# Kernel tuning notes

Hardware: AMD Instinct MI355X
Metric: run time of the kernel (lower is better)

Reference implementation:

```python
import jax, jax.numpy as jnp
import numpy as np

N = 100000      # nodes
E = 1600000     # edges (avg degree 16)
F_IN = 128      # dataset.num_features
H = 64          # hidden_channels
C = 40          # dataset.num_classes
LAYERS = 4      # number_conv_layers
EPS = 1e-12     # F.normalize eps


def _agnn_layer(x, src, dst):
    # AGNNConv with beta=1 (requires_grad=False):
    # alpha_ij = softmax_i( cos(x_i, x_j) ), out_i = sum_j alpha_ij * x_j
    xn = x / jnp.maximum(jnp.linalg.norm(x, axis=1, keepdims=True), EPS)
    logits = jnp.sum(xn[dst] * xn[src], axis=1)                      # [E]
    m = jax.lax.stop_gradient(jax.ops.segment_max(logits, dst, num_segments=N))
    e = jnp.exp(logits - m[dst])
    s = jax.ops.segment_sum(e, dst, num_segments=N)
    alpha = e / s[dst]                                               # [E]
    return jax.ops.segment_sum(alpha[:, None] * x[src], dst, num_segments=N)


def setup_inputs() -> dict:
    key = jax.random.key(0)
    k = jax.random.split(key, 6)
    x = jax.random.normal(k[0], (N, F_IN), dtype=jnp.float32)
    edge_index = jax.random.randint(k[1], (2, E), 0, N, dtype=jnp.int32)
    W1 = jax.random.normal(k[2], (F_IN, H), dtype=jnp.float32) * (1.0 / np.sqrt(F_IN))
    b1 = jnp.zeros((H,), dtype=jnp.float32)
    W2 = jax.random.normal(k[3], (H, C), dtype=jnp.float32) * (1.0 / np.sqrt(H))
    b2 = jnp.zeros((C,), dtype=jnp.float32)
    return {"x": x, "W1": W1, "b1": b1, "W2": W2, "b2": b2, "edge_index": edge_index}


def reference(x, W1, b1, W2, b2, edge_index):
    # add self loops (PyG AGNNConv default)
    loop = jnp.arange(N, dtype=edge_index.dtype)
    src = jnp.concatenate([edge_index[0], loop])
    dst = jnp.concatenate([edge_index[1], loop])
    h = jax.nn.relu(x @ W1 + b1)          # lin1 + relu (dropout p=0 / eval)
    for _ in range(LAYERS):
        h = _agnn_layer(h, src, dst)
    out = h @ W2 + b2                     # lin2
    return jax.nn.log_softmax(out, axis=1)
```

## Files before the change

kernel.cpp:

```cpp
#include <hip/hip_runtime.h>
#include <math.h>

#define F_IN 128
#define H_DIM 64
#define C_OUT 40
#define NBK 391
#define CHUNK 4096
#define XPAD 136
#define PHB 128

typedef _Float16 h8 __attribute__((ext_vector_type(8)));
typedef _Float16 half2t __attribute__((ext_vector_type(2)));
typedef float nf4 __attribute__((ext_vector_type(4)));
typedef _Float16 f16x8 __attribute__((ext_vector_type(8)));
typedef float f32x4 __attribute__((ext_vector_type(4)));

union H8 {
    h8 v;
    half2t p[4];
};

__device__ __forceinline__ float dot8(const H8& a, const H8& b) {
    float d = __builtin_amdgcn_fdot2(a.p[0], b.p[0], 0.0f, false);
    d = __builtin_amdgcn_fdot2(a.p[1], b.p[1], d, false);
    d = __builtin_amdgcn_fdot2(a.p[2], b.p[2], d, false);
    d = __builtin_amdgcn_fdot2(a.p[3], b.p[3], d, false);
    return d;
}

__device__ __forceinline__ float dpp_red8_add(float x) {
    int v = __builtin_bit_cast(int, x);
    x += __builtin_bit_cast(float, __builtin_amdgcn_update_dpp(0, v, 0xB1, 0xF, 0xF, true));
    v = __builtin_bit_cast(int, x);
    x += __builtin_bit_cast(float, __builtin_amdgcn_update_dpp(0, v, 0x4E, 0xF, 0xF, true));
    v = __builtin_bit_cast(int, x);
    x += __builtin_bit_cast(float, __builtin_amdgcn_update_dpp(0, v, 0x141, 0xF, 0xF, true));
    return x;
}


__global__ void __launch_bounds__(256) bphist_kernel(const int* __restrict__ dst,
                                                     int* __restrict__ part, int E) {
    __shared__ int lh[512];
    int tid = threadIdx.x;
    lh[tid] = 0; lh[tid + 256] = 0;
    __syncthreads();
    int slice = (E + PHB - 1) / PHB;
    int lo = blockIdx.x * slice;
    int hi = min(E, lo + slice);
    for (int e = lo + tid; e < hi; e += 256) {
        int d = __builtin_nontemporal_load(&dst[e]);
        atomicAdd(&lh[d >> 8], 1);
    }
    __syncthreads();
    part[blockIdx.x * 512 + tid] = lh[tid];
    part[blockIdx.x * 512 + tid + 256] = lh[tid + 256];
}

__global__ void __launch_bounds__(512) bscan_kernel(const int* __restrict__ part,
                                                    int* __restrict__ bbase,
                                                    int* __restrict__ bcursor, int E) {
    __shared__ int sa[512], sb[512];
    int t = threadIdx.x;
    int v = 0;
#pragma unroll 4
    for (int b = 0; b < PHB; b++) v += part[b * 512 + t];
    sa[t] = v;
    __syncthreads();
    int* pa = sa; int* pb = sb;
#pragma unroll
    for (int off = 1; off < 512; off <<= 1) {
        pb[t] = pa[t] + ((t >= off) ? pa[t - off] : 0);
        __syncthreads();
        int* tmp = pa; pa = pb; pb = tmp;
    }
    if (t < NBK) {
        int excl = pa[t] - v;
        bbase[t] = excl;
        bcursor[t] = excl;
    }
    if (t == 0) bbase[NBK] = E;
}

__global__ void __launch_bounds__(256) binscatter_kernel(const int* __restrict__ src,
                                                         const int* __restrict__ dst,
                                                         int* __restrict__ bcursor,
                                                         unsigned int* __restrict__ pairs, int E) {
    __shared__ unsigned int sp[CHUNK];
    __shared__ unsigned short sbof[CHUNK];
    __shared__ int hist[512];
    __shared__ int scanA[512], scanB[512];
    __shared__ int cur[512];
    __shared__ int gbase[512];
    int tid = threadIdx.x;
    int e0 = blockIdx.x * CHUNK;
    int cnt = min(CHUNK, E - e0);

    int dv[CHUNK / 256], sv[CHUNK / 256];
#pragma unroll
    for (int i = 0; i < CHUNK / 256; i++) {
        int idx = tid + i * 256;
        if (idx < cnt) {
            dv[i] = __builtin_nontemporal_load(&dst[e0 + idx]);
            sv[i] = __builtin_nontemporal_load(&src[e0 + idx]);
        }
    }
    hist[tid] = 0; hist[tid + 256] = 0;
    __syncthreads();
#pragma unroll
    for (int i = 0; i < CHUNK / 256; i++) {
        int idx = tid + i * 256;
        if (idx < cnt) atomicAdd(&hist[dv[i] >> 8], 1);
    }
    __syncthreads();
    scanA[tid] = hist[tid]; scanA[tid + 256] = hist[tid + 256];
    __syncthreads();
    int* pa = scanA; int* pb = scanB;
#pragma unroll
    for (int off = 1; off < 512; off <<= 1) {
        pb[tid] = pa[tid] + ((tid >= off) ? pa[tid - off] : 0);
        int t1 = tid + 256;
        pb[t1] = pa[t1] + ((t1 >= off) ? pa[t1 - off] : 0);
        __syncthreads();
        int* tmp = pa; pa = pb; pb = tmp;
    }
    cur[tid] = pa[tid] - hist[tid];
    cur[tid + 256] = pa[tid + 256] - hist[tid + 256];
    __syncthreads();
#pragma unroll
    for (int i = 0; i < CHUNK / 256; i++) {
        int idx = tid + i * 256;
        if (idx < cnt) {
            int b = dv[i] >> 8;
            int lp = atomicAdd(&cur[b], 1);
            sp[lp] = ((unsigned int)(dv[i] & 255) << 24) | (unsigned int)sv[i];
            sbof[lp] = (unsigned short)b;
        }
    }
    {
        int c0 = hist[tid];
        gbase[tid] = c0 ? atomicAdd(&bcursor[tid], c0) : 0;
        int c1 = hist[tid + 256];
        gbase[tid + 256] = c1 ? atomicAdd(&bcursor[tid + 256], c1) : 0;
    }
    __syncthreads();
    for (int i = tid; i < cnt; i += 256) {
        int b = sbof[i];
        int off_in_b = i - (pa[b] - hist[b]);
        pairs[gbase[b] + off_in_b] = sp[i];
    }
}

__global__ void __launch_bounds__(256) bucketsort_kernel(const unsigned int* __restrict__ pairs,
                                                         const int* __restrict__ bbase,
                                                         int* __restrict__ rowptr,
                                                         int* __restrict__ ssrc, int N, int E) {
    __shared__ int hist[256], scanA[256], scanB[256], cur[256];
    int b = blockIdx.x;
    int tid = threadIdx.x;
    int e0 = bbase[b], e1 = bbase[b + 1];
    hist[tid] = 0;
    __syncthreads();
    for (int e = e0 + tid; e < e1; e += 256) {
        unsigned int p = pairs[e];
        atomicAdd(&hist[p >> 24], 1);
    }
    __syncthreads();
    scanA[tid] = hist[tid];
    __syncthreads();
    int* pa = scanA; int* pb = scanB;
#pragma unroll
    for (int off = 1; off < 256; off <<= 1) {
        pb[tid] = pa[tid] + ((tid >= off) ? pa[tid - off] : 0);
        __syncthreads();
        int* tmp = pa; pa = pb; pb = tmp;
    }
    int excl = pa[tid] - hist[tid];
    int node = (b << 8) + tid;
    if (node < N) rowptr[node] = e0 + excl;
    if (b == NBK - 1 && tid == 0) rowptr[N] = E;
    cur[tid] = e0 + excl;
    __syncthreads();
    for (int e = e0 + tid; e < e1; e += 256) {
        unsigned int p = pairs[e];
        int pos = atomicAdd(&cur[p >> 24], 1);
        ssrc[pos] = (int)(p & 0x00FFFFFFu);
    }
}

__global__ void __launch_bounds__(256) cvtw_kernel(const float* __restrict__ W1,
                                                   _Float16* __restrict__ w1t) {
    int t = blockIdx.x * 256 + threadIdx.x;
    if (t < F_IN * H_DIM) {
        int k = t >> 6, col = t & 63;
        w1t[col * F_IN + k] = (_Float16)W1[t];
    }
}

__global__ void __launch_bounds__(256) lin1_kernel(
        const float* __restrict__ x, const _Float16* __restrict__ w1t,
        const float* __restrict__ b1, _Float16* __restrict__ hnout,
        float* __restrict__ nrmout, int n) {
    __shared__ _Float16 sx[64 * XPAD];
    __shared__ _Float16 sw[64 * XPAD];
    int tid = threadIdx.x;
    int r0 = blockIdx.x * 64;

    for (int ch = tid; ch < 64 * 32; ch += 256) {
        int row = ch >> 5, k4 = (ch & 31) << 2;
        float4 xv = make_float4(0.f, 0.f, 0.f, 0.f);
        if (r0 + row < n) xv = *(const float4*)(x + (size_t)(r0 + row) * F_IN + k4);
        _Float16* p = &sx[row * XPAD + k4];
        p[0] = (_Float16)xv.x; p[1] = (_Float16)xv.y;
        p[2] = (_Float16)xv.z; p[3] = (_Float16)xv.w;
    }
    for (int ch = tid; ch < 64 * 16; ch += 256) {
        int col = ch >> 4, k8 = (ch & 15) << 3;
        *(uint4*)&sw[col * XPAD + k8] = *(const uint4*)(w1t + col * F_IN + k8);
    }
    __syncthreads();

    int w = tid >> 6, lane = tid & 63;
    int q = lane >> 4, c = lane & 15;

    f16x8 afrag[4];
#pragma unroll
    for (int kk = 0; kk < 4; kk++)
        afrag[kk] = *(const f16x8*)&sx[(w * 16 + c) * XPAD + kk * 32 + q * 8];

    f32x4 acc[4] = {{0.f,0.f,0.f,0.f},{0.f,0.f,0.f,0.f},{0.f,0.f,0.f,0.f},{0.f,0.f,0.f,0.f}};
#pragma unroll
    for (int ct = 0; ct < 4; ct++) {
#pragma unroll
        for (int kk = 0; kk < 4; kk++) {
            f16x8 bfrag = *(const f16x8*)&sw[(ct * 16 + c) * XPAD + kk * 32 + q * 8];
            acc[ct] = __builtin_amdgcn_mfma_f32_16x16x32_f16(afrag[kk], bfrag, acc[ct], 0, 0, 0);
        }
    }

    float ss[4] = {0.f, 0.f, 0.f, 0.f};
#pragma unroll
    for (int ct = 0; ct < 4; ct++) {
        float bv = b1[ct * 16 + c];
#pragma unroll
        for (int r = 0; r < 4; r++) {
            float v = fmaxf(acc[ct][r] + bv, 0.0f);
            acc[ct][r] = v;
            ss[r] = fmaf(v, v, ss[r]);
        }
    }
#pragma unroll
    for (int k = 1; k < 16; k <<= 1) {
#pragma unroll
        for (int r = 0; r < 4; r++) ss[r] += __shfl_xor(ss[r], k, 64);
    }
    float nn[4], inv[4];
#pragma unroll
    for (int r = 0; r < 4; r++) {
        nn[r] = fmaxf(sqrtf(ss[r]), 1e-12f);
        inv[r] = 1.0f / nn[r];
    }
#pragma unroll
    for (int ct = 0; ct < 4; ct++)
#pragma unroll
        for (int r = 0; r < 4; r++)
            sx[(w * 16 + q * 4 + r) * XPAD + ct * 16 + c] = (_Float16)(acc[ct][r] * inv[r]);

    if (c == 0) {
#pragma unroll
        for (int r = 0; r < 4; r++) {
            int row = r0 + w * 16 + q * 4 + r;
            if (row < n) nrmout[row] = nn[r];
        }
    }
#pragma unroll
    for (int it = 0; it < 2; it++) {
        int row = w * 16 + it * 8 + (lane >> 3);
        int k8 = (lane & 7) * 8;
        if (r0 + row < n)
            *(uint4*)(hnout + (size_t)(r0 + row) * H_DIM + k8) =
                *(const uint4*)&sx[row * XPAD + k8];
    }
}

__global__ void __launch_bounds__(256, 3) agnn_kernel(
        const h8* __restrict__ h, const float* __restrict__ nrm,
        const int* __restrict__ rowptr, const int* __restrict__ ssrc,
        h8* __restrict__ hout, float* __restrict__ nrmout, int n, int E) {
    int wv = (blockIdx.x * blockDim.x + threadIdx.x) >> 6;
    int lane = threadIdx.x & 63;
    int g = lane >> 3;
    int sub = lane & 7;
    int wid = wv * 8 + g;
    bool nvalid = wid < n;
    int nid = nvalid ? wid : (n - 1);

    int e0 = rowptr[nid];
    int e1 = rowptr[nid + 1];
    int steps = nvalid ? (e1 - e0) : 0;
    int eclamp = min(max(e1 - 1, e0), E - 1);

    H8 hd; hd.v = h[(size_t)nid * 8 + sub];
    float ni = nrm[nid];

    int mx = steps;
    mx = max(mx, __shfl_xor(mx, 8, 64));
    mx = max(mx, __shfl_xor(mx, 16, 64));
    mx = max(mx, __shfl_xor(mx, 32, 64));

    float dself = dpp_red8_add(dot8(hd, hd));
    float wself = __expf(dself);
    float sw = wself;
    float aself = wself * ni;
    half2t ap = {(_Float16)aself, (_Float16)aself};
    half2t acc2[4];
#pragma unroll
    for (int j = 0; j < 4; j++) acc2[j] = ap * hd.p[j];

    int sA[8], sB[8];
    H8 XA[8], XB[8];
    float nA[8], nB[8];

    auto SLOAD = [&](int* s, int ofs) {
#pragma unroll
        for (int k = 0; k < 8; k++) s[k] = ssrc[min(e0 + ofs + k, eclamp)];
    };
    auto HLOAD = [&](const int* s, H8* X, float* xn) {
#pragma unroll
        for (int k = 0; k < 8; k++) {
            X[k].v = h[(size_t)s[k] * 8 + sub];
            xn[k] = nrm[s[k]];
        }
    };
    auto COMP = [&](const H8* X, const float* xn, int base) {
        float d[8];
#pragma unroll
        for (int k = 0; k < 8; k++) d[k] = dpp_red8_add(dot8(X[k], hd));
#pragma unroll
        for (int k = 0; k < 8; k++) {
            float wgt = (base + k < steps) ? __expf(d[k]) : 0.0f;
            sw += wgt;
            float a = wgt * xn[k];
            half2t apk = {(_Float16)a, (_Float16)a};
#pragma unroll
            for (int j = 0; j < 4; j++) acc2[j] += apk * X[k].p[j];
        }
    };

    int nb = (mx + 7) >> 3;
    SLOAD(sA, 0);
    __builtin_amdgcn_sched_barrier(0);
    HLOAD(sA, XA, nA);
    SLOAD(sB, 8);
    __builtin_amdgcn_sched_barrier(0);

    int base = 0;
    for (int b = 0; b < nb; b += 2) {
        HLOAD(sB, XB, nB);
        SLOAD(sA, base + 16);
        __builtin_amdgcn_sched_barrier(0);
        COMP(XA, nA, base);
        __builtin_amdgcn_sched_barrier(0);
        if (b + 1 >= nb) break;
        HLOAD(sA, XA, nA);
        SLOAD(sB, base + 24);
        __builtin_amdgcn_sched_barrier(0);
        COMP(XB, nB, base + 8);
        __builtin_amdgcn_sched_barrier(0);
        base += 16;
    }

    float inv = 1.0f / sw;
    float o[8];
#pragma unroll
    for (int j = 0; j < 4; j++) {
        o[2 * j] = (float)acc2[j][0] * inv;
        o[2 * j + 1] = (float)acc2[j][1] * inv;
    }
    float ss = 0.0f;
#pragma unroll
    for (int i = 0; i < 8; i++) ss = fmaf(o[i], o[i], ss);
    ss = dpp_red8_add(ss);
    float nn = fmaxf(sqrtf(ss), 1e-12f);
    float r = 1.0f / nn;
    h8 oh;
#pragma unroll
    for (int i = 0; i < 8; i++) oh[i] = (_Float16)(o[i] * r);
    if (nvalid) {
        hout[(size_t)wid * 8 + sub] = oh;
        if (sub == 0) nrmout[wid] = nn;
    }
}

__global__ void __launch_bounds__(256) lin2_kernel(
        const h8* __restrict__ h, const float* __restrict__ nrm,
        const float* __restrict__ W2, const float* __restrict__ b2,
        float* __restrict__ out, int n) {
    __shared__ h8 sh[32 * 8];
    __shared__ float snrm[32];
    int tid = threadIdx.x;
    int r0 = blockIdx.x * 32;
    int rows = min(32, n - r0);

    {
        const uint4* hg = (const uint4*)(h + (size_t)r0 * 8);
        uint4* sh4 = (uint4*)sh;
        int tot = rows * 8;
        for (int i = tid; i < tot; i += 256) sh4[i] = hg[i];
        if (tid < rows) snrm[tid] = nrm[r0 + tid];
    }
    __syncthreads();

    int wave = tid >> 6, lane = tid & 63;
    int rbase = wave * 8;

    float acc[8];
    if (lane < C_OUT) {
#pragma unroll
        for (int j = 0; j < 8; j++) acc[j] = 0.0f;
#pragma unroll 2
        for (int k = 0; k < H_DIM; k += 8) {
            float w[8];
#pragma unroll
            for (int i = 0; i < 8; i++) w[i] = W2[(k + i) * C_OUT + lane];
#pragma unroll
            for (int j = 0; j < 8; j++) {
                h8 hv = sh[(rbase + j) * 8 + (k >> 3)];
#pragma unroll
                for (int i = 0; i < 8; i++) acc[j] = fmaf((float)hv[i], w[i], acc[j]);
            }
        }
        float bl = b2[lane];
#pragma unroll
        for (int j = 0; j < 8; j++) acc[j] = fmaf(snrm[rbase + j], acc[j], bl);
    } else {
#pragma unroll
        for (int j = 0; j < 8; j++) acc[j] = -INFINITY;
    }

#pragma unroll
    for (int j = 0; j < 8; j++) {
        int r = rbase + j;
        if (r >= rows) break;
        float m = acc[j];
#pragma unroll
        for (int k = 1; k < 64; k <<= 1) m = fmaxf(m, __shfl_xor(m, k, 64));
        float e = (lane < C_OUT) ? __expf(acc[j] - m) : 0.0f;
        float s = e;
#pragma unroll
        for (int k = 1; k < 64; k <<= 1) s += __shfl_xor(s, k, 64);
        if (lane < C_OUT) out[(size_t)(r0 + r) * C_OUT + lane] = acc[j] - m - logf(s);
    }
}


extern "C" void kernel_launch(void* const* d_in, const int* in_sizes, int n_in,
                              void* d_out, int out_size, void* d_ws, size_t ws_size,
                              hipStream_t stream) {
    const float* x = (const float*)d_in[0];
    const float* W1 = (const float*)d_in[1];
    const float* b1 = (const float*)d_in[2];
    const float* W2 = (const float*)d_in[3];
    const float* b2 = (const float*)d_in[4];
    const int* ei = (const int*)d_in[5];

    const int N = in_sizes[0] / F_IN;
    const int E = in_sizes[5] / 2;
    const int* src = ei;
    const int* dst = ei + E;

    char* w = (char*)d_ws;
    auto carve = [&](size_t bytes) {
        char* p = w;
        w += (bytes + 255) & ~(size_t)255;
        return p;
    };
    _Float16* g1 = (_Float16*)carve((size_t)N * H_DIM * 2);
    _Float16* g2 = (_Float16*)carve((size_t)N * H_DIM * 2);
    float* rn1 = (float*)carve((size_t)N * 4);
    float* rn2 = (float*)carve((size_t)N * 4);
    int* rowptr = (int*)carve((size_t)(N + 1) * 4);
    int* bbase = (int*)carve(512 * 4);
    int* bcursor = (int*)carve(512 * 4);
    int* ssrc = (int*)carve((size_t)E * 4);
    _Float16* w1t = (_Float16*)carve((size_t)F_IN * H_DIM * 2);
    unsigned int* pairs = (unsigned int*)g2;
    int* part = (int*)g1;

    bphist_kernel<<<PHB, 256, 0, stream>>>(dst, part, E);
    bscan_kernel<<<1, 512, 0, stream>>>(part, bbase, bcursor, E);
    binscatter_kernel<<<(E + CHUNK - 1) / CHUNK, 256, 0, stream>>>(src, dst, bcursor, pairs, E);
    bucketsort_kernel<<<NBK, 256, 0, stream>>>(pairs, bbase, rowptr, ssrc, N, E);

    cvtw_kernel<<<(F_IN * H_DIM + 255) / 256, 256, 0, stream>>>(W1, w1t);
    lin1_kernel<<<(N + 63) / 64, 256, 0, stream>>>(x, w1t, b1, g1, rn1, N);

    {
        int blocks = (N + 31) / 32;
        agnn_kernel<<<blocks, 256, 0, stream>>>((const h8*)g1, rn1, rowptr, ssrc, (h8*)g2, rn2, N, E);
        agnn_kernel<<<blocks, 256, 0, stream>>>((const h8*)g2, rn2, rowptr, ssrc, (h8*)g1, rn1, N, E);
        agnn_kernel<<<blocks, 256, 0, stream>>>((const h8*)g1, rn1, rowptr, ssrc, (h8*)g2, rn2, N, E);
        agnn_kernel<<<blocks, 256, 0, stream>>>((const h8*)g2, rn2, rowptr, ssrc, (h8*)g1, rn1, N, E);
    }

    lin2_kernel<<<(N + 31) / 32, 256, 0, stream>>>((const h8*)g1, rn1, W2, b2, (float*)d_out, N);
}
```

Baseline: 246.5 us.

## Fold weight conversion into histogram kernel and stage bucket pairs in LDS

Removes the separate W1 conversion launch by handling it in extra blocks of the histogram kernel. The bin-scatter kernel now runs with 512 threads on smaller 2048-edge chunks, giving more blocks and one histogram bin per thread. The bucket sort uses 512 threads and caches each bucket's pairs in shared memory when they fit, so the second pass reads LDS instead of global memory. The risks are higher LDS use per block, lower occupancy, and a fallback path for oversized buckets.

Result: no change. 248.6 us (+0.8%).

```diff
diff --git a/kernel.cpp b/kernel.cpp
--- a/kernel.cpp
+++ b/kernel.cpp
@@ -5,9 +5,10 @@
 #define H_DIM 64
 #define C_OUT 40
 #define NBK 391
-#define CHUNK 4096
+#define CHUNK 2048
 #define XPAD 136
 #define PHB 128
+#define BCAP 5120
 
 typedef _Float16 h8 __attribute__((ext_vector_type(8)));
 typedef _Float16 half2t __attribute__((ext_vector_type(2)));
@@ -40,7 +41,17 @@
 
 
 __global__ void __launch_bounds__(256) bphist_kernel(const int* __restrict__ dst,
-                                                     int* __restrict__ part, int E) {
+                                                     int* __restrict__ part, int E,
+                                                     const float* __restrict__ W1,
+                                                     _Float16* __restrict__ w1t) {
+    if (blockIdx.x >= PHB) {
+        int t = (blockIdx.x - PHB) * 256 + threadIdx.x;
+        if (t < F_IN * H_DIM) {
+            int k = t >> 6, col = t & 63;
+            w1t[col * F_IN + k] = (_Float16)W1[t];
+        }
+        return;
+    }
     __shared__ int lh[512];
     int tid = threadIdx.x;
     lh[tid] = 0; lh[tid + 256] = 0;
@@ -82,7 +93,7 @@
     if (t == 0) bbase[NBK] = E;
 }
 
-__global__ void __launch_bounds__(256) binscatter_kernel(const int* __restrict__ src,
+__global__ void __launch_bounds__(512) binscatter_kernel(const int* __restrict__ src,
                                                          const int* __restrict__ dst,
                                                          int* __restrict__ bcursor,
                                                          unsigned int* __restrict__ pairs, int E) {
@@ -96,40 +107,37 @@
     int e0 = blockIdx.x * CHUNK;
     int cnt = min(CHUNK, E - e0);
 
-    int dv[CHUNK / 256], sv[CHUNK / 256];
-#pragma unroll
-    for (int i = 0; i < CHUNK / 256; i++) {
-        int idx = tid + i * 256;
+    int dv[CHUNK / 512], sv[CHUNK / 512];
+#pragma unroll
+    for (int i = 0; i < CHUNK / 512; i++) {
+        int idx = tid + i * 512;
         if (idx < cnt) {
             dv[i] = __builtin_nontemporal_load(&dst[e0 + idx]);
             sv[i] = __builtin_nontemporal_load(&src[e0 + idx]);
         }
     }
-    hist[tid] = 0; hist[tid + 256] = 0;
-    __syncthreads();
-#pragma unroll
-    for (int i = 0; i < CHUNK / 256; i++) {
-        int idx = tid + i * 256;
+    hist[tid] = 0;
+    __syncthreads();
+#pragma unroll
+    for (int i = 0; i < CHUNK / 512; i++) {
+        int idx = tid + i * 512;
         if (idx < cnt) atomicAdd(&hist[dv[i] >> 8], 1);
     }
     __syncthreads();
-    scanA[tid] = hist[tid]; scanA[tid + 256] = hist[tid + 256];
+    scanA[tid] = hist[tid];
     __syncthreads();
     int* pa = scanA; int* pb = scanB;
 #pragma unroll
     for (int off = 1; off < 512; off <<= 1) {
         pb[tid] = pa[tid] + ((tid >= off) ? pa[tid - off] : 0);
-        int t1 = tid + 256;
-        pb[t1] = pa[t1] + ((t1 >= off) ? pa[t1 - off] : 0);
         __syncthreads();
         int* tmp = pa; pa = pb; pb = tmp;
     }
     cur[tid] = pa[tid] - hist[tid];
-    cur[tid + 256] = pa[tid + 256] - hist[tid + 256];
-    __syncthreads();
-#pragma unroll
-    for (int i = 0; i < CHUNK / 256; i++) {
-        int idx = tid + i * 256;
+    __syncthreads();
+#pragma unroll
+    for (int i = 0; i < CHUNK / 512; i++) {
+        int idx = tid + i * 512;
         if (idx < cnt) {
             int b = dv[i] >> 8;
             int lp = atomicAdd(&cur[b], 1);
@@ -140,60 +148,58 @@
     {
         int c0 = hist[tid];
         gbase[tid] = c0 ? atomicAdd(&bcursor[tid], c0) : 0;
-        int c1 = hist[tid + 256];
-        gbase[tid + 256] = c1 ? atomicAdd(&bcursor[tid + 256], c1) : 0;
-    }
-    __syncthreads();
-    for (int i = tid; i < cnt; i += 256) {
+    }
+    __syncthreads();
+    for (int i = tid; i < cnt; i += 512) {
         int b = sbof[i];
         int off_in_b = i - (pa[b] - hist[b]);
         pairs[gbase[b] + off_in_b] = sp[i];
     }
 }
 
-__global__ void __launch_bounds__(256) bucketsort_kernel(const unsigned int* __restrict__ pairs,
+__global__ void __launch_bounds__(512) bucketsort_kernel(const unsigned int* __restrict__ pairs,
                                                          const int* __restrict__ bbase,
                                                          int* __restrict__ rowptr,
                                                          int* __restrict__ ssrc, int N, int E) {
+    __shared__ unsigned int spairs[BCAP];
     __shared__ int hist[256], scanA[256], scanB[256], cur[256];
     int b = blockIdx.x;
     int tid = threadIdx.x;
     int e0 = bbase[b], e1 = bbase[b + 1];
-    hist[tid] = 0;
-    __syncthreads();
-    for (int e = e0 + tid; e < e1; e += 256) {
-        unsigned int p = pairs[e];
+    int cnt = e1 - e0;
+    bool lds = cnt <= BCAP;
+
+    if (tid < 256) hist[tid] = 0;
+    if (lds) {
+        for (int i = tid; i < cnt; i += 512) spairs[i] = pairs[e0 + i];
+    }
+    __syncthreads();
+    for (int i = tid; i < cnt; i += 512) {
+        unsigned int p = lds ? spairs[i] : pairs[e0 + i];
         atomicAdd(&hist[p >> 24], 1);
     }
     __syncthreads();
-    scanA[tid] = hist[tid];
+    if (tid < 256) scanA[tid] = hist[tid];
     __syncthreads();
     int* pa = scanA; int* pb = scanB;
 #pragma unroll
     for (int off = 1; off < 256; off <<= 1) {
-        pb[tid] = pa[tid] + ((tid >= off) ? pa[tid - off] : 0);
+        if (tid < 256) pb[tid] = pa[tid] + ((tid >= off) ? pa[tid - off] : 0);
         __syncthreads();
         int* tmp = pa; pa = pb; pb = tmp;
     }
-    int excl = pa[tid] - hist[tid];
-    int node = (b << 8) + tid;
-    if (node < N) rowptr[node] = e0 + excl;
+    if (tid < 256) {
+        int excl = pa[tid] - hist[tid];
+        int node = (b << 8) + tid;
+        if (node < N) rowptr[node] = e0 + excl;
+        cur[tid] = e0 + excl;
+    }
     if (b == NBK - 1 && tid == 0) rowptr[N] = E;
-    cur[tid] = e0 + excl;
-    __syncthreads();
-    for (int e = e0 + tid; e < e1; e += 256) {
-        unsigned int p = pairs[e];
+    __syncthreads();
+    for (int i = tid; i < cnt; i += 512) {
+        unsigned int p = lds ? spairs[i] : pairs[e0 + i];
         int pos = atomicAdd(&cur[p >> 24], 1);
         ssrc[pos] = (int)(p & 0x00FFFFFFu);
-    }
-}
-
-__global__ void __launch_bounds__(256) cvtw_kernel(const float* __restrict__ W1,
-                                                   _Float16* __restrict__ w1t) {
-    int t = blockIdx.x * 256 + threadIdx.x;
-    if (t < F_IN * H_DIM) {
-        int k = t >> 6, col = t & 63;
-        w1t[col * F_IN + k] = (_Float16)W1[t];
     }
 }
 
@@ -487,12 +493,11 @@
     unsigned int* pairs = (unsigned int*)g2;
     int* part = (int*)g1;
 
-    bphist_kernel<<<PHB, 256, 0, stream>>>(dst, part, E);
+    bphist_kernel<<<PHB + 32, 256, 0, stream>>>(dst, part, E, W1, w1t);
     bscan_kernel<<<1, 512, 0, stream>>>(part, bbase, bcursor, E);
-    binscatter_kernel<<<(E + CHUNK - 1) / CHUNK, 256, 0, stream>>>(src, dst, bcursor, pairs, E);
-    bucketsort_kernel<<<NBK, 256, 0, stream>>>(pairs, bbase, rowptr, ssrc, N, E);
-
-    cvtw_kernel<<<(F_IN * H_DIM + 255) / 256, 256, 0, stream>>>(W1, w1t);
+    binscatter_kernel<<<(E + CHUNK - 1) / CHUNK, 512, 0, stream>>>(src, dst, bcursor, pairs, E);
+    bucketsort_kernel<<<NBK, 512, 0, stream>>>(pairs, bbase, rowptr, ssrc, N, E);
+
     lin1_kernel<<<(N + 63) / 64, 256, 0, stream>>>(x, w1t, b1, g1, rn1, N);
 
     {
```
